# Optimization experiments

Hardware: AMD Instinct MI355X
Metric: run time of the kernel (lower is better)

The kernel has to match this reference:

```python
import jax, jax.numpy as jnp
import numpy as np

B, S, D, H = 16, 577, 1408, 16
HD = D // H  # 88


def setup_inputs() -> dict:
    key = jax.random.key(0)
    k1, k2, k3, k4, k5, k6 = jax.random.split(key, 6)
    hidden_states = jax.random.normal(k1, (B, S, D), dtype=jnp.float32)
    # realistic rotary table: cos/sin pairs stacked in last dim
    theta = jax.random.normal(k2, (S, HD // 2), dtype=jnp.float32)
    freqs_ci = jnp.stack([jnp.cos(theta), jnp.sin(theta)], axis=-1)  # (S, HD/2, 2)
    wqkv = jax.random.normal(k3, (3 * D, D), dtype=jnp.float32) * 0.02
    bqkv = jax.random.normal(k4, (3 * D,), dtype=jnp.float32) * 0.02
    wo = jax.random.normal(k5, (D, D), dtype=jnp.float32) * 0.02
    bo = jax.random.normal(k6, (D,), dtype=jnp.float32) * 0.02
    return {"hidden_states": hidden_states, "freqs_ci": freqs_ci,
            "wqkv": wqkv, "bqkv": bqkv, "wo": wo, "bo": bo}


def reference(hidden_states, freqs_ci, wqkv, bqkv, wo, bo):
    b, s, d = hidden_states.shape
    # fused QKV projection (torch Linear: x @ W.T + b)
    qkv = hidden_states @ wqkv.T + bqkv  # (B, S, 3D)
    q, k, v = jnp.split(qkv, 3, axis=-1)
    q = q.reshape(b, s, H, HD)
    k = k.reshape(b, s, H, HD)
    v = v.reshape(b, s, H, HD)

    cos = freqs_ci[..., 0][None, :, None, :]  # (1, S, 1, HD/2)
    sin = freqs_ci[..., 1][None, :, None, :]

    def rot(x):
        xr = x.reshape(b, s, H, HD // 2, 2)
        xe, xo = xr[..., 0], xr[..., 1]
        re = xe * cos - xo * sin
        ro = xe * sin + xo * cos
        return jnp.stack([re, ro], axis=-1).reshape(b, s, H, HD)

    q = rot(q)
    k = rot(k)

    scale = 1.0 / jnp.sqrt(jnp.float32(HD))  # SDPA default scaling
    scores = jnp.einsum('bqhd,bkhd->bhqk', q, k) * scale
    attn = jax.nn.softmax(scores, axis=-1)
    ctx = jnp.einsum('bhqk,bkhd->bqhd', attn, v).reshape(b, s, d)
    return ctx @ wo.T + bo
```

## Files before the change

### kernel.cpp

```cpp
#include <hip/hip_runtime.h>

typedef __attribute__((ext_vector_type(8))) __bf16 bf16x8;
typedef __attribute__((ext_vector_type(4))) float f32x4;
typedef __attribute__((ext_vector_type(4))) unsigned int uint4v;

#define B_ 16
#define S_ 577
#define D_ 1408
#define H_ 16
#define HD_ 88
#define MROWS (B_*S_)
#define N1 (3*D_)
#define K_ D_
#define VT_LD 592
#define SCALE 0.10660035817780521f

static __device__ __forceinline__ void async16(void* lds, const void* g) {
  __builtin_amdgcn_global_load_lds((const __attribute__((address_space(1))) void*)g,
                                   (__attribute__((address_space(3))) void*)lds, 16, 0, 0);
}

static __device__ __forceinline__ int xcd_swizzle(int orig, int nwg) {
  int xcd = orig & 7, lid = orig >> 3;
  int q = nwg >> 3, r = nwg & 7;
  return (xcd < r ? xcd * (q + 1) : r * (q + 1) + (xcd - r) * q) + lid;
}

#define LGKM0() do { asm volatile("s_waitcnt lgkmcnt(0)" ::: "memory"); \
                     __builtin_amdgcn_sched_barrier(0); } while (0)
#define VMDRAIN() asm volatile("s_waitcnt vmcnt(0)" ::: "memory")
#define BARR() __builtin_amdgcn_s_barrier()

__global__ void cast_bf16_kernel(const float* __restrict__ src, __bf16* __restrict__ dst, int n4) {
  int i = blockIdx.x * blockDim.x + threadIdx.x;
  if (i >= n4) return;
  const float4 v = ((const float4*)src)[i];
  __bf16* d = dst + (size_t)i * 4;
  d[0] = (__bf16)v.x; d[1] = (__bf16)v.y; d[2] = (__bf16)v.z; d[3] = (__bf16)v.w;
}

__device__ __forceinline__ void gemm256_core(const __bf16* __restrict__ A,
                                             const __bf16* __restrict__ Bm,
                                             int m0, int n0, int Arows, int Brows,
                                             __bf16* lds, f32x4 (&acc)[8][4]) {
  const int tid = threadIdx.x;
  const int w = tid >> 6, l = tid & 63;
  const int wm = w >> 2, wn = w & 3;
  const int l15 = l & 15;
  const int x0 = (((l >> 4) * 8)) ^ ((l & 7) << 3);
  const int x1 = ((32 + (l >> 4) * 8)) ^ ((l & 7) << 3);
  const int sbase = w * 512;

  const int lr = w * 8 + (l >> 3);
  const int swc = ((l & 7) ^ (l >> 3)) * 8;
  const __bf16* pa[2][2];
  const __bf16* pb[2][2];
#pragma unroll
  for (int h = 0; h < 2; ++h)
#pragma unroll
    for (int r8 = 0; r8 < 2; ++r8) {
      int ra = m0 + h * 128 + r8 * 64 + lr; if (ra >= Arows) ra = Arows - 1;
      int rb = n0 + h * 128 + r8 * 64 + lr; if (rb >= Brows) rb = Brows - 1;
      pa[h][r8] = A + (size_t)ra * K_ + swc;
      pb[h][r8] = Bm + (size_t)rb * K_ + swc;
    }

#pragma unroll
  for (int m = 0; m < 8; ++m)
#pragma unroll
    for (int n = 0; n < 4; ++n) acc[m][n] = (f32x4){0.f, 0.f, 0.f, 0.f};

#pragma unroll
  for (int h = 0; h < 2; ++h)
#pragma unroll
    for (int r8 = 0; r8 < 2; ++r8) {
      async16(lds + h * 8192 + r8 * 4096 + sbase, pa[h][r8]);
      async16(lds + 16384 + h * 8192 + r8 * 4096 + sbase, pb[h][r8]);
    }
  VMDRAIN();
  BARR();

  bf16x8 af[4][2], bfr[2][2];

#define RD_A(MH) { _Pragma("unroll") for (int i = 0; i < 4; ++i) { \
    const __bf16* rp = At + (wm * 128 + (MH) * 64 + i * 16 + l15) * 64; \
    af[i][0] = *(const bf16x8*)(rp + x0); af[i][1] = *(const bf16x8*)(rp + x1); } }
#define RD_B(NH) { _Pragma("unroll") for (int jn = 0; jn < 2; ++jn) { \
    const __bf16* rp = Bt + (wn * 64 + (NH) * 32 + jn * 16 + l15) * 64; \
    bfr[jn][0] = *(const bf16x8*)(rp + x0); bfr[jn][1] = *(const bf16x8*)(rp + x1); } }
#define MM(MH, NH) { __builtin_amdgcn_s_setprio(1); \
    _Pragma("unroll") for (int i = 0; i < 4; ++i) _Pragma("unroll") for (int jn = 0; jn < 2; ++jn) { \
      acc[(MH)*4+i][(NH)*2+jn] = __builtin_amdgcn_mfma_f32_16x16x32_bf16(af[i][0], bfr[jn][0], acc[(MH)*4+i][(NH)*2+jn], 0, 0, 0); \
      acc[(MH)*4+i][(NH)*2+jn] = __builtin_amdgcn_mfma_f32_16x16x32_bf16(af[i][1], bfr[jn][1], acc[(MH)*4+i][(NH)*2+jn], 0, 0, 0); } \
    __builtin_amdgcn_s_setprio(0); }
#define STG(WHICH, PP, KC) { _Pragma("unroll") for (int h = 0; h < 2; ++h) \
    _Pragma("unroll") for (int r8 = 0; r8 < 2; ++r8) \
      async16(Sd + (WHICH) * 16384 + h * 8192 + r8 * 4096 + sbase, PP[h][r8] + (KC)); }

  for (int kt = 0; kt < 21; ++kt) {
    __bf16* At = lds + (kt & 1) * 32768;
    __bf16* Bt = At + 16384;
    __bf16* Sd = lds + ((kt & 1) ^ 1) * 32768;
    const int kc = (kt + 1) * 64;
    RD_A(0); RD_B(0);
    STG(0, pa, kc);
    BARR(); LGKM0();
    MM(0, 0);
    BARR();
    RD_A(1);
    STG(1, pb, kc);
    BARR(); LGKM0();
    MM(1, 0);
    BARR();
    RD_B(1);
    BARR(); LGKM0();
    MM(1, 1);
    BARR();
    RD_A(0);
    BARR(); LGKM0();
    MM(0, 1);
    VMDRAIN();
    BARR();
  }
  {
    __bf16* At = lds + 32768;
    __bf16* Bt = At + 16384;
    RD_A(0); RD_B(0);
    BARR(); LGKM0();
    MM(0, 0);
    BARR();
    RD_A(1);
    BARR(); LGKM0();
    MM(1, 0);
    BARR();
    RD_B(1);
    BARR(); LGKM0();
    MM(1, 1);
    BARR();
    RD_A(0);
    BARR(); LGKM0();
    MM(0, 1);
  }
#undef RD_A
#undef RD_B
#undef MM
#undef STG
}

__launch_bounds__(512, 2)
__global__ void gemm_qkv_rope(const __bf16* __restrict__ A, const __bf16* __restrict__ Bm,
                              const float* __restrict__ bias, const float* __restrict__ freqs,
                              __bf16* __restrict__ Qb, __bf16* __restrict__ Kb,
                              __bf16* __restrict__ Vb) {
  __shared__ __align__(16) __bf16 lds[65536];
  const int wgid = xcd_swizzle(blockIdx.x, 37 * 17);
  const int m0 = (wgid % 37) * 256, n0 = (wgid / 37) * 256;
  f32x4 acc[8][4];
  gemm256_core(A, Bm, m0, n0, MROWS, N1, lds, acc);

  const int tid = threadIdx.x;
  const int w = tid >> 6, l = tid & 63;
  const int wm = w >> 2, wn = w & 3;
#pragma unroll
  for (int n = 0; n < 4; ++n) {
    const int col = n0 + wn * 64 + n * 16 + (l & 15);
    if (col >= N1) continue;
    const int sect = col / 1408;
    const int cin = col - sect * 1408;
    const int h = cin / 88, d = cin - h * 88;
    const float bv = bias[col];
    const float sgn = (d & 1) ? 1.f : -1.f;
    const int i2 = d & ~1;
    __bf16* dst = (sect == 0) ? Qb : (sect == 1 ? Kb : Vb);
#pragma unroll
    for (int m = 0; m < 8; ++m) {
      const int rb = m0 + wm * 128 + m * 16 + (l >> 4) * 4;
#pragma unroll
      for (int j = 0; j < 4; ++j) {
        const int r = rb + j;
        float val = acc[m][n][j] + bv;
        const int s = r % 577;
        float outv = val;
        if (sect < 2) {
          const float2 cs = *(const float2*)&freqs[s * 88 + i2];
          const float p = __shfl_xor(val, 1);
          outv = val * cs.x + sgn * p * cs.y;
        }
        if (r < MROWS) {
          const int b = r / 577;
          dst[((size_t)(b * 16 + h) * 577 + s) * 88 + d] = (__bf16)outv;
        }
      }
    }
  }
}

__launch_bounds__(512, 2)
__global__ void gemm_out_bias(const __bf16* __restrict__ A, const __bf16* __restrict__ Bm,
                              const float* __restrict__ bias, float* __restrict__ C) {
  __shared__ __align__(16) __bf16 lds[65536];
  const int wgid = xcd_swizzle(blockIdx.x, 37 * 6);
  const int m0 = (wgid % 37) * 256, n0 = (wgid / 37) * 256;
  f32x4 acc[8][4];
  gemm256_core(A, Bm, m0, n0, MROWS, D_, lds, acc);

  const int tid = threadIdx.x;
  const int w = tid >> 6, l = tid & 63;
  const int wm = w >> 2, wn = w & 3;
#pragma unroll
  for (int n = 0; n < 4; ++n) {
    const int col = n0 + wn * 64 + n * 16 + (l & 15);
    if (col >= D_) continue;
    const float bv = bias[col];
#pragma unroll
    for (int m = 0; m < 8; ++m) {
      const int rb = m0 + wm * 128 + m * 16 + (l >> 4) * 4;
#pragma unroll
      for (int j = 0; j < 4; ++j) {
        const int r = rb + j;
        if (r < MROWS) C[(size_t)r * D_ + col] = acc[m][n][j] + bv;
      }
    }
  }
}

__global__ void transpose_v(const __bf16* __restrict__ V, __bf16* __restrict__ Vt_g) {
  __shared__ __bf16 Ls[64 * 104];
  const int bh = blockIdx.x, t = blockIdx.y, s0 = t * 64;
  const int tid = threadIdx.x;
  const __bf16* vp = V + (size_t)bh * 577 * 88;
  for (int i = tid; i < 64 * 11; i += 256) {
    int r = i / 11, off = i % 11;
    int gs = s0 + r; if (gs > 576) gs = 576;
    *(uint4v*)&Ls[r * 104 + off * 8] = *(const uint4v*)(vp + (size_t)gs * 88 + off * 8);
  }
  __syncthreads();
  for (int i = tid; i < 88 * 8; i += 256) {
    int d = i / 8, so = (i % 8) * 8;
    int sc_ = s0 + so;
    if (sc_ < VT_LD) {
      __bf16 tmp[8];
#pragma unroll
      for (int j = 0; j < 8; ++j) tmp[j] = Ls[(so + j) * 104 + d];
      *(uint4v*)&Vt_g[((size_t)bh * 88 + d) * VT_LD + sc_] = *(uint4v*)tmp;
    }
  }
}

__launch_bounds__(256, 3)
__global__ void attn_kernel(const __bf16* __restrict__ Q, const __bf16* __restrict__ K,
                            const __bf16* __restrict__ Vt_gp, __bf16* __restrict__ ctx) {
  __shared__ __bf16 lds[26368];
  const int tid = threadIdx.x;
  const int w = tid >> 6, l = tid & 63;
  const int bh = blockIdx.x;
  const int q0 = blockIdx.y * 128;
  const __bf16* qp = Q + (size_t)bh * 577 * 88;
  const __bf16* kp = K + (size_t)bh * 577 * 88;
  const __bf16* vtp = Vt_gp + (size_t)bh * 88 * VT_LD;
  __bf16* Qs = lds;
  __bf16* Ks = lds + 12288;
  __bf16* Vt = lds + 17920;
  __bf16* Pw = lds + w * 2304;

  for (int i = tid; i < 128 * 11; i += 256) {
    int r = i / 11, off = i % 11;
    int gr = q0 + r; if (gr > 576) gr = 576;
    *(uint4v*)&Qs[r * 96 + off * 8] = *(const uint4v*)(qp + (size_t)gr * 88 + off * 8);
  }
  if (tid < 128) { uint4v z = 0; *(uint4v*)&Qs[tid * 96 + 88] = z; }
  __syncthreads();

  bf16x8 qf[2][3];
#pragma unroll
  for (int mg = 0; mg < 2; ++mg)
#pragma unroll
    for (int kk = 0; kk < 3; ++kk)
      qf[mg][kk] = *(const bf16x8*)&Qs[(w * 32 + mg * 16 + (l & 15)) * 96 + kk * 32 + (l >> 4) * 8];

  int preA[7], preB[7];
#pragma unroll
  for (int kch = 0; kch < 7; ++kch) {
    int c = w + 4 * kch;
    int a = 0, b2 = 0;
    if (c < 11) a = c * 512 + l * 8;
    else if (c < 27) { int e = (c - 11) * 512 + l * 8; a = (e / 88) * VT_LD; b2 = e % 88; }
    preA[kch] = a; preB[kch] = b2;
  }

  f32x4 oacc[2][6];
#pragma unroll
  for (int mg = 0; mg < 2; ++mg)
#pragma unroll
    for (int dn = 0; dn < 6; ++dn) oacc[mg][dn] = (f32x4){0.f, 0.f, 0.f, 0.f};
  f32x4 mrun[2], lrun[2];
  mrun[0] = -1e30f; mrun[1] = -1e30f;
  lrun[0] = 0.f; lrun[1] = 0.f;

  for (int t = 0; t < 10; ++t) {
    const int s0 = t * 64;
    if (t) __syncthreads();
#pragma unroll
    for (int kch = 0; kch < 7; ++kch) {
      int c = w + 4 * kch;
      if (c < 11) {
        async16(Ks + c * 512, kp + (size_t)s0 * 88 + preA[kch]);
      } else if (c < 27) {
        int g = s0 + preB[kch]; if (g > 584) g = 584;
        async16(Vt + (c - 11) * 512, vtp + preA[kch] + g);
      }
    }
    __syncthreads();

    f32x4 sc[2][4];
#pragma unroll
    for (int mg = 0; mg < 2; ++mg)
#pragma unroll
      for (int n = 0; n < 4; ++n) sc[mg][n] = (f32x4){0.f, 0.f, 0.f, 0.f};
#pragma unroll
    for (int n = 0; n < 4; ++n) {
#pragma unroll
      for (int kk = 0; kk < 3; ++kk) {
        bf16x8 kf = *(const bf16x8*)&Ks[(n * 16 + (l & 15)) * 88 + kk * 32 + (l >> 4) * 8];
        sc[0][n] = __builtin_amdgcn_mfma_f32_16x16x32_bf16(qf[0][kk], kf, sc[0][n], 0, 0, 0);
        sc[1][n] = __builtin_amdgcn_mfma_f32_16x16x32_bf16(qf[1][kk], kf, sc[1][n], 0, 0, 0);
      }
    }

    f32x4 tmax[2];
    tmax[0] = -1e30f; tmax[1] = -1e30f;
#pragma unroll
    for (int n = 0; n < 4; ++n) {
      const int kc = s0 + n * 16 + (l & 15);
      const bool valid = kc < 577;
#pragma unroll
      for (int mg = 0; mg < 2; ++mg)
#pragma unroll
        for (int j = 0; j < 4; ++j) {
          float v = valid ? sc[mg][n][j] * SCALE : -1e30f;
          sc[mg][n][j] = v;
          tmax[mg][j] = fmaxf(tmax[mg][j], v);
        }
    }
#pragma unroll
    for (int o = 1; o < 16; o <<= 1)
#pragma unroll
      for (int mg = 0; mg < 2; ++mg)
#pragma unroll
        for (int j = 0; j < 4; ++j)
          tmax[mg][j] = fmaxf(tmax[mg][j], __shfl_xor(tmax[mg][j], o));
#pragma unroll
    for (int mg = 0; mg < 2; ++mg)
#pragma unroll
      for (int j = 0; j < 4; ++j) {
        float mo = mrun[mg][j];
        float mn = fmaxf(mo, tmax[mg][j]);
        float sf = __expf(mo - mn);
        mrun[mg][j] = mn;
        lrun[mg][j] *= sf;
#pragma unroll
        for (int dn = 0; dn < 6; ++dn) oacc[mg][dn][j] *= sf;
      }
#pragma unroll
    for (int mg = 0; mg < 2; ++mg)
#pragma unroll
      for (int n = 0; n < 4; ++n)
#pragma unroll
        for (int j = 0; j < 4; ++j) {
          float p = __expf(sc[mg][n][j] - mrun[mg][j]);
          lrun[mg][j] += p;
          Pw[(mg * 16 + (l >> 4) * 4 + j) * 72 + n * 16 + (l & 15)] = (__bf16)p;
        }

#pragma unroll
    for (int ks = 0; ks < 2; ++ks) {
      bf16x8 pa0 = *(const bf16x8*)&Pw[((l & 15)) * 72 + ks * 32 + (l >> 4) * 8];
      bf16x8 pa1 = *(const bf16x8*)&Pw[(16 + (l & 15)) * 72 + ks * 32 + (l >> 4) * 8];
#pragma unroll
      for (int dn = 0; dn < 6; ++dn) {
        bf16x8 vb = *(const bf16x8*)&Vt[(dn * 16 + (l & 15)) * 88 + ks * 32 + (l >> 4) * 8];
        oacc[0][dn] = __builtin_amdgcn_mfma_f32_16x16x32_bf16(pa0, vb, oacc[0][dn], 0, 0, 0);
        oacc[1][dn] = __builtin_amdgcn_mfma_f32_16x16x32_bf16(pa1, vb, oacc[1][dn], 0, 0, 0);
      }
    }
  }

#pragma unroll
  for (int o = 1; o < 16; o <<= 1)
#pragma unroll
    for (int mg = 0; mg < 2; ++mg)
#pragma unroll
      for (int j = 0; j < 4; ++j)
        lrun[mg][j] += __shfl_xor(lrun[mg][j], o);

  const int b = bh >> 4, h = bh & 15;
#pragma unroll
  for (int mg = 0; mg < 2; ++mg) {
    float inv[4];
#pragma unroll
    for (int j = 0; j < 4; ++j) inv[j] = 1.f / lrun[mg][j];
    const int sqb = q0 + w * 32 + mg * 16 + (l >> 4) * 4;
#pragma unroll
    for (int dn = 0; dn < 6; ++dn) {
      const int d = dn * 16 + (l & 15);
      if (d >= 88) continue;
#pragma unroll
      for (int j = 0; j < 4; ++j) {
        const int sq = sqb + j;
        if (sq < 577)
          ctx[((size_t)(b * 577 + sq)) * 1408 + h * 88 + d] = (__bf16)(oacc[mg][dn][j] * inv[j]);
      }
    }
  }
}

extern "C" void kernel_launch(void* const* d_in, const int* in_sizes, int n_in,
                              void* d_out, int out_size, void* d_ws, size_t ws_size,
                              hipStream_t stream) {
  const float* hs    = (const float*)d_in[0];
  const float* freqs = (const float*)d_in[1];
  const float* wqkv  = (const float*)d_in[2];
  const float* bqkv  = (const float*)d_in[3];
  const float* wo    = (const float*)d_in[4];
  const float* bo    = (const float*)d_in[5];
  float* out = (float*)d_out;

  char* ws = (char*)d_ws;
  size_t off = 0;
  auto alloc = [&](size_t bytes) {
    void* p = ws + off;
    off += (bytes + 255) & ~(size_t)255;
    return p;
  };
  __bf16* x_bf    = (__bf16*)alloc((size_t)MROWS * K_ * 2);
  __bf16* ctx_bf  = x_bf;
  __bf16* wqkv_bf = (__bf16*)alloc((size_t)N1 * K_ * 2);
  __bf16* wo_bf   = (__bf16*)alloc((size_t)D_ * K_ * 2);
  __bf16* q_bf    = (__bf16*)alloc((size_t)MROWS * D_ * 2);
  __bf16* k_bf    = (__bf16*)alloc((size_t)MROWS * D_ * 2);
  __bf16* v_bf    = (__bf16*)alloc((size_t)MROWS * D_ * 2);
  __bf16* vt_g    = (__bf16*)d_out;

  cast_bf16_kernel<<<(MROWS * K_ / 4 + 255) / 256, 256, 0, stream>>>(hs, x_bf, MROWS * K_ / 4);
  cast_bf16_kernel<<<(N1 * K_ / 4 + 255) / 256, 256, 0, stream>>>(wqkv, wqkv_bf, N1 * K_ / 4);
  cast_bf16_kernel<<<(D_ * K_ / 4 + 255) / 256, 256, 0, stream>>>(wo, wo_bf, D_ * K_ / 4);

  gemm_qkv_rope<<<37 * 17, 512, 0, stream>>>(x_bf, wqkv_bf, bqkv, freqs, q_bf, k_bf, v_bf);

  transpose_v<<<dim3(256, 10), 256, 0, stream>>>(v_bf, vt_g);

  attn_kernel<<<dim3(256, 5), 256, 0, stream>>>(q_bf, k_bf, vt_g, ctx_bf);

  gemm_out_bias<<<37 * 6, 512, 0, stream>>>(ctx_bf, wo_bf, bo, out);
}
```

Measured before the change: 422.9 us.

## Restructure GEMM main loop into half-tile staged pipeline with partial vmcnt waits

Rewrites the shared 256x256 bf16 GEMM core so each 128-row/col half of the A and B tiles is prefetched separately, up to two k-steps ahead, and half-tiles are reused in LDS slots as soon as they are consumed. Full vmcnt(0) drains are replaced with vmcnt(4) waits, and the wave-to-tile mapping changes so each wave owns interleaved 64x32 sub-blocks within the two halves. The epilogues are updated to match the new mapping. The aim is to keep global loads in flight across MFMA phases and shorten stalls at barriers, at the cost of more complex hazard ordering that relies on careful barrier placement.

```diff
diff --git a/kernel.cpp b/kernel.cpp
--- a/kernel.cpp
+++ b/kernel.cpp
@@ -26,10 +26,11 @@
   return (xcd < r ? xcd * (q + 1) : r * (q + 1) + (xcd - r) * q) + lid;
 }
 
-#define LGKM0() do { asm volatile("s_waitcnt lgkmcnt(0)" ::: "memory"); \
-                     __builtin_amdgcn_sched_barrier(0); } while (0)
+#define SB0() __builtin_amdgcn_sched_barrier(0)
+#define LGKM0() do { asm volatile("s_waitcnt lgkmcnt(0)" ::: "memory"); SB0(); } while (0)
+#define VMW4()  do { asm volatile("s_waitcnt vmcnt(4)" ::: "memory"); SB0(); } while (0)
 #define VMDRAIN() asm volatile("s_waitcnt vmcnt(0)" ::: "memory")
-#define BARR() __builtin_amdgcn_s_barrier()
+#define BARR() do { SB0(); __builtin_amdgcn_s_barrier(); SB0(); } while (0)
 
 __global__ void cast_bf16_kernel(const float* __restrict__ src, __bf16* __restrict__ dst, int n4) {
   int i = blockIdx.x * blockDim.x + threadIdx.x;
@@ -47,8 +48,8 @@
   const int w = tid >> 6, l = tid & 63;
   const int wm = w >> 2, wn = w & 3;
   const int l15 = l & 15;
-  const int x0 = (((l >> 4) * 8)) ^ ((l & 7) << 3);
-  const int x1 = ((32 + (l >> 4) * 8)) ^ ((l & 7) << 3);
+  const int x0 = ((l >> 4) * 8) ^ ((l & 7) << 3);
+  const int x1 = (32 + (l >> 4) * 8) ^ ((l & 7) << 3);
   const int sbase = w * 512;
 
   const int lr = w * 8 + (l >> 3);
@@ -70,81 +71,62 @@
 #pragma unroll
     for (int n = 0; n < 4; ++n) acc[m][n] = (f32x4){0.f, 0.f, 0.f, 0.f};
 
-#pragma unroll
-  for (int h = 0; h < 2; ++h)
-#pragma unroll
-    for (int r8 = 0; r8 < 2; ++r8) {
-      async16(lds + h * 8192 + r8 * 4096 + sbase, pa[h][r8]);
-      async16(lds + 16384 + h * 8192 + r8 * 4096 + sbase, pb[h][r8]);
-    }
-  VMDRAIN();
-  BARR();
-
   bf16x8 af[4][2], bfr[2][2];
 
-#define RD_A(MH) { _Pragma("unroll") for (int i = 0; i < 4; ++i) { \
-    const __bf16* rp = At + (wm * 128 + (MH) * 64 + i * 16 + l15) * 64; \
+#define STG_A(DB, H, KC) { async16(lds + (DB)*32768 + (H)*8192 + sbase, pa[H][0] + (KC)); \
+                           async16(lds + (DB)*32768 + (H)*8192 + 4096 + sbase, pa[H][1] + (KC)); }
+#define STG_B(DB, H, KC) { async16(lds + (DB)*32768 + 16384 + (H)*8192 + sbase, pb[H][0] + (KC)); \
+                           async16(lds + (DB)*32768 + 16384 + (H)*8192 + 4096 + sbase, pb[H][1] + (KC)); }
+#define RD_A(DB, MH) { _Pragma("unroll") for (int i = 0; i < 4; ++i) { \
+    const __bf16* rp = lds + (DB)*32768 + ((MH) * 128 + wm * 64 + i * 16 + l15) * 64; \
     af[i][0] = *(const bf16x8*)(rp + x0); af[i][1] = *(const bf16x8*)(rp + x1); } }
-#define RD_B(NH) { _Pragma("unroll") for (int jn = 0; jn < 2; ++jn) { \
-    const __bf16* rp = Bt + (wn * 64 + (NH) * 32 + jn * 16 + l15) * 64; \
+#define RD_B(DB, NH) { _Pragma("unroll") for (int jn = 0; jn < 2; ++jn) { \
+    const __bf16* rp = lds + (DB)*32768 + 16384 + ((NH) * 128 + wn * 32 + jn * 16 + l15) * 64; \
     bfr[jn][0] = *(const bf16x8*)(rp + x0); bfr[jn][1] = *(const bf16x8*)(rp + x1); } }
 #define MM(MH, NH) { __builtin_amdgcn_s_setprio(1); \
     _Pragma("unroll") for (int i = 0; i < 4; ++i) _Pragma("unroll") for (int jn = 0; jn < 2; ++jn) { \
       acc[(MH)*4+i][(NH)*2+jn] = __builtin_amdgcn_mfma_f32_16x16x32_bf16(af[i][0], bfr[jn][0], acc[(MH)*4+i][(NH)*2+jn], 0, 0, 0); \
       acc[(MH)*4+i][(NH)*2+jn] = __builtin_amdgcn_mfma_f32_16x16x32_bf16(af[i][1], bfr[jn][1], acc[(MH)*4+i][(NH)*2+jn], 0, 0, 0); } \
     __builtin_amdgcn_s_setprio(0); }
-#define STG(WHICH, PP, KC) { _Pragma("unroll") for (int h = 0; h < 2; ++h) \
-    _Pragma("unroll") for (int r8 = 0; r8 < 2; ++r8) \
-      async16(Sd + (WHICH) * 16384 + h * 8192 + r8 * 4096 + sbase, PP[h][r8] + (KC)); }
-
-  for (int kt = 0; kt < 21; ++kt) {
-    __bf16* At = lds + (kt & 1) * 32768;
-    __bf16* Bt = At + 16384;
-    __bf16* Sd = lds + ((kt & 1) ^ 1) * 32768;
-    const int kc = (kt + 1) * 64;
-    RD_A(0); RD_B(0);
-    STG(0, pa, kc);
+
+  STG_A(0, 0, 0); STG_B(0, 0, 0); STG_B(0, 1, 0); STG_A(0, 1, 0);
+  SB0();
+  STG_A(1, 0, 64); STG_B(1, 1, 64);
+  VMW4();
+  BARR();
+
+  for (int u = 0; u < 22; ++u) {
+    const int DB = u & 1, OD = DB ^ 1;
+    const int kcN  = (u + 1 < 22) ? (u + 1) * 64 : 0;
+    const int kcNN = (u + 2 < 22) ? (u + 2) * 64 : 0;
+    RD_A(DB, 0); RD_B(DB, 0);
+    STG_A(OD, 1, kcN);
     BARR(); LGKM0();
     MM(0, 0);
     BARR();
-    RD_A(1);
-    STG(1, pb, kc);
+    RD_B(DB, 1);
+    STG_B(OD, 0, kcN);
     BARR(); LGKM0();
-    MM(1, 0);
+    MM(0, 1);
     BARR();
-    RD_B(1);
+    RD_A(DB, 1);
+    STG_A(DB, 0, kcNN);
     BARR(); LGKM0();
     MM(1, 1);
     BARR();
-    RD_A(0);
-    BARR(); LGKM0();
-    MM(0, 1);
-    VMDRAIN();
-    BARR();
-  }
-  {
-    __bf16* At = lds + 32768;
-    __bf16* Bt = At + 16384;
-    RD_A(0); RD_B(0);
-    BARR(); LGKM0();
-    MM(0, 0);
-    BARR();
-    RD_A(1);
+    RD_B(DB, 0);
+    STG_B(DB, 1, kcNN);
     BARR(); LGKM0();
     MM(1, 0);
+    VMW4();
     BARR();
-    RD_B(1);
-    BARR(); LGKM0();
-    MM(1, 1);
-    BARR();
-    RD_A(0);
-    BARR(); LGKM0();
-    MM(0, 1);
-  }
+  }
+  VMDRAIN();
+#undef STG_A
+#undef STG_B
 #undef RD_A
 #undef RD_B
 #undef MM
-#undef STG
 }
 
 __launch_bounds__(512, 2)
@@ -163,7 +145,7 @@
   const int wm = w >> 2, wn = w & 3;
 #pragma unroll
   for (int n = 0; n < 4; ++n) {
-    const int col = n0 + wn * 64 + n * 16 + (l & 15);
+    const int col = n0 + (n >> 1) * 128 + wn * 32 + (n & 1) * 16 + (l & 15);
     if (col >= N1) continue;
     const int sect = col / 1408;
     const int cin = col - sect * 1408;
@@ -174,7 +156,7 @@
     __bf16* dst = (sect == 0) ? Qb : (sect == 1 ? Kb : Vb);
 #pragma unroll
     for (int m = 0; m < 8; ++m) {
-      const int rb = m0 + wm * 128 + m * 16 + (l >> 4) * 4;
+      const int rb = m0 + (m >> 2) * 128 + wm * 64 + (m & 3) * 16 + (l >> 4) * 4;
 #pragma unroll
       for (int j = 0; j < 4; ++j) {
         const int r = rb + j;
@@ -209,12 +191,12 @@
   const int wm = w >> 2, wn = w & 3;
 #pragma unroll
   for (int n = 0; n < 4; ++n) {
-    const int col = n0 + wn * 64 + n * 16 + (l & 15);
+    const int col = n0 + (n >> 1) * 128 + wn * 32 + (n & 1) * 16 + (l & 15);
     if (col >= D_) continue;
     const float bv = bias[col];
 #pragma unroll
     for (int m = 0; m < 8; ++m) {
-      const int rb = m0 + wm * 128 + m * 16 + (l >> 4) * 4;
+      const int rb = m0 + (m >> 2) * 128 + wm * 64 + (m & 3) * 16 + (l >> 4) * 4;
 #pragma unroll
       for (int j = 0; j < 4; ++j) {
         const int r = rb + j;
```

Result: no change. 421.5 us (-0.3%).
